# Kernel tuning notes

Hardware: AMD Instinct MI355X
Metric: run time of the kernel (lower is better)

Reference implementation:

```python
import jax, jax.numpy as jnp
import numpy as np

N, E, D, L, G = 100000, 320000, 256, 3, 4096
EPS = 1e-5


def setup_inputs() -> dict:
    key = jax.random.key(0)
    ks = jax.random.split(key, 14)
    s = 0.05
    return {
        "x": jax.random.normal(ks[0], (N, D), jnp.float32),
        "lin1_w": jax.random.normal(ks[1], (L, D, D), jnp.float32) * s,
        "lin1_b": jnp.zeros((L, D), jnp.float32),
        "lin2_w": jax.random.normal(ks[2], (L, D, D), jnp.float32) * s,
        "lin2_b": jnp.zeros((L, D), jnp.float32),
        "bn_g": jnp.ones((L, D), jnp.float32),
        "bn_b": jnp.zeros((L, D), jnp.float32),
        "gru_wih": jax.random.normal(ks[3], (L, 3 * D, D), jnp.float32) * s,
        "gru_whh": jax.random.normal(ks[4], (L, 3 * D, D), jnp.float32) * s,
        "gru_bih": jnp.zeros((L, 3 * D), jnp.float32),
        "gru_bhh": jnp.zeros((L, 3 * D), jnp.float32),
        "ln_g": jnp.ones((D,), jnp.float32),
        "ln_b": jnp.zeros((D,), jnp.float32),
        "edge_index": jax.random.randint(ks[5], (2, E), 0, N),
        "batch": jnp.sort(jax.random.randint(ks[6], (N,), 0, G)),
    }


def _layer_norm(h, g, b):
    mu = jnp.mean(h, axis=-1, keepdims=True)
    var = jnp.mean(jnp.square(h - mu), axis=-1, keepdims=True)
    return (h - mu) * jax.lax.rsqrt(var + EPS) * g + b


def _batch_norm(h, g, b):
    mu = jnp.mean(h, axis=0)
    var = jnp.mean(jnp.square(h - mu), axis=0)
    return (h - mu) * jax.lax.rsqrt(var + EPS) * g + b


def reference(x, lin1_w, lin1_b, lin2_w, lin2_b, bn_g, bn_b,
              gru_wih, gru_whh, gru_bih, gru_bhh, ln_g, ln_b,
              edge_index, batch):
    src, dst = edge_index[0], edge_index[1]
    h = x
    m = jnp.ones((), x.dtype)   # running elementwise product (starts as scalar 1)
    e = jnp.zeros((), x.dtype)  # running elementwise sum (starts as scalar 0)
    hs = []
    for i in range(L):
        # GIN aggregation: (1+eps)*h + sum_{j->i} h_j, eps=0
        agg = jax.ops.segment_sum(h[src], dst, num_segments=N) + h
        # GIN MLP: Linear -> ReLU -> Linear, then outer ReLU
        t = jax.nn.relu(agg @ lin1_w[i].T + lin1_b[i])
        t = t @ lin2_w[i].T + lin2_b[i]
        g = jax.nn.relu(t)
        g = _batch_norm(g, bn_g[i], bn_b[i])  # dropout is identity in eval
        # GRUCell(input=g, hidden=h)
        gi = g @ gru_wih[i].T + gru_bih[i]
        gh = h @ gru_whh[i].T + gru_bhh[i]
        i_r, i_z, i_n = jnp.split(gi, 3, axis=-1)
        h_r, h_z, h_n = jnp.split(gh, 3, axis=-1)
        r = jax.nn.sigmoid(i_r + h_r)
        z = jax.nn.sigmoid(i_z + h_z)
        n = jnp.tanh(i_n + r * h_n)
        h = (1.0 - z) * n + z * h
        h = _layer_norm(h, ln_g, ln_b)
        m = m * h
        e = e + h
        hs.append(h)
    node_rep = jnp.concatenate(hs + [m, e], axis=-1)  # [N, (L+2)*D]
    out = jax.ops.segment_max(node_rep, batch, num_segments=G)  # [G, (L+2)*D]
    return out
```

## Files before the change

kernel.cpp:

```cpp
#include <hip/hip_runtime.h>

#define N_NODES 100000
#define N_EDGES 320000
#define N_GRAPH 4096
#define M_PAD   100096
#define N_TILES 782
#define LN_EPS  1e-5f
#define S_EL    ((size_t)M_PAD * 256)
#define CAP     32

typedef __attribute__((ext_vector_type(8))) short short8;
typedef __attribute__((ext_vector_type(4))) float f32x4;
typedef unsigned short u16;

__device__ __forceinline__ float bf2f(u16 u){
  return __uint_as_float(((unsigned)u) << 16);
}
__device__ __forceinline__ u16 f2bf(float f){
  unsigned u = __float_as_uint(f);
  return (u16)((u + 0x7FFFu + ((u >> 16) & 1u)) >> 16);
}
__device__ __forceinline__ float ldext(const void* p, long i, bool f32){
  return f32 ? ((const float*)p)[i] : bf2f(((const u16*)p)[i]);
}
__device__ __forceinline__ float fsigm(float x){
  return __builtin_amdgcn_rcpf(1.0f + __expf(-x));
}
__device__ __forceinline__ float ftanh(float x){
  float cx = fminf(fmaxf(x, -15.f), 15.f);
  return 1.0f - 2.0f*__builtin_amdgcn_rcpf(__expf(2.0f*cx) + 1.0f);
}

__device__ __forceinline__ int swzb(int row, int colByte){
  return (row << 9) + (colByte ^ ((row & 7) << 4));
}

__global__ void k_detect(const unsigned* __restrict__ x32, int* __restrict__ flag){
  unsigned u = x32[threadIdx.x];
  int ef = (int)((u >> 23) & 0xFFu);
  int ok = (ef >= 64 && ef <= 190) ? 1 : 0;
  #pragma unroll
  for (int o=1; o<64; o<<=1) ok += __shfl_xor(ok, o);
  if (threadIdx.x == 0) *flag = (ok >= 32) ? 1 : 0;
}

__global__ void k_wconv(const void* __restrict__ src, u16* __restrict__ dst,
                        const int* __restrict__ dflag){
  const bool f32 = (*dflag != 0);
  size_t base = ((size_t)blockIdx.x*256 + threadIdx.x)*8;
  if (f32){
    const float* s = (const float*)src + base;
    float4 a = *(const float4*)s;
    float4 b = *(const float4*)(s + 4);
    ushort4 lo = make_ushort4(f2bf(a.x),f2bf(a.y),f2bf(a.z),f2bf(a.w));
    ushort4 hi = make_ushort4(f2bf(b.x),f2bf(b.y),f2bf(b.z),f2bf(b.w));
    uint4 v;
    v.x = (unsigned)lo.x | ((unsigned)lo.y<<16);
    v.y = (unsigned)lo.z | ((unsigned)lo.w<<16);
    v.z = (unsigned)hi.x | ((unsigned)hi.y<<16);
    v.w = (unsigned)hi.z | ((unsigned)hi.w<<16);
    *(uint4*)&dst[base] = v;
  } else {
    *(uint4*)&dst[base] = *(const uint4*)((const u16*)src + base);
  }
}

__global__ void k_h_init(const void* __restrict__ x, u16* __restrict__ h,
                         const int* __restrict__ dflag){
  const bool f32 = (*dflag != 0);
  int i = blockIdx.x*256 + threadIdx.x;
  size_t base = (size_t)i*8;
  int n = (int)(base >> 8);
  uint4 v = make_uint4(0,0,0,0);
  if (n < N_NODES){
    if (f32){
      const float* xf = (const float*)x + base;
      float4 a = *(const float4*)xf;
      float4 b = *(const float4*)(xf + 4);
      ushort4 lo = make_ushort4(f2bf(a.x),f2bf(a.y),f2bf(a.z),f2bf(a.w));
      ushort4 hi = make_ushort4(f2bf(b.x),f2bf(b.y),f2bf(b.z),f2bf(b.w));
      v.x = (unsigned)lo.x | ((unsigned)lo.y<<16);
      v.y = (unsigned)lo.z | ((unsigned)lo.w<<16);
      v.z = (unsigned)hi.x | ((unsigned)hi.y<<16);
      v.w = (unsigned)hi.z | ((unsigned)hi.w<<16);
    } else {
      v = *(const uint4*)((const u16*)x + base);
    }
  }
  *(uint4*)&h[base] = v;
}

__global__ void k_bucket_build(const int* __restrict__ ei, int* __restrict__ cnt,
                               int* __restrict__ bucket, int* __restrict__ ovf,
                               int* __restrict__ ovfcnt){
  int e = blockIdx.x*256 + threadIdx.x;
  if (e >= N_EDGES) return;
  int s = ei[e];
  int d = ei[N_EDGES + e];
  int pos = atomicAdd(&cnt[d], 1);
  if (pos < CAP) bucket[(size_t)d*CAP + pos] = s;
  else { int o = atomicAdd(ovfcnt, 1); ovf[o] = e; }
}

__global__ __launch_bounds__(256) void k_gather(
    const unsigned* __restrict__ h32, const int* __restrict__ cnt,
    const int* __restrict__ bucket, unsigned* __restrict__ G32)
{
  int gid = blockIdx.x*256 + threadIdx.x;
  int n = gid >> 7;
  int j = gid & 127;
  unsigned hv = h32[(size_t)n*128 + j];
  float lo = bf2f((u16)(hv & 0xFFFFu));
  float hi = bf2f((u16)(hv >> 16));
  int c = (n < N_NODES) ? min(cnt[n], CAP) : 0;
  const int* bk = &bucket[(size_t)n*CAP];
  for (int k = 0; k < c; k++){
    int s = bk[k];
    unsigned v = h32[(size_t)s*128 + j];
    lo += bf2f((u16)(v & 0xFFFFu));
    hi += bf2f((u16)(v >> 16));
  }
  G32[(size_t)n*128 + j] = (unsigned)f2bf(lo) | ((unsigned)f2bf(hi) << 16);
}

__global__ void k_ovf_scatter(const unsigned* __restrict__ h32,
                              const int* __restrict__ ei,
                              const int* __restrict__ ovf,
                              const int* __restrict__ ovfcnt,
                              unsigned* __restrict__ G32){
  const long work = (long)(*ovfcnt) * 128;
  for (long i = (long)blockIdx.x*256 + threadIdx.x; i < work;
       i += (long)gridDim.x*256){
    int e = ovf[i >> 7];
    int j = (int)(i & 127);
    int s = ei[e];
    int d = ei[N_EDGES + e];
    unsigned sv = h32[(size_t)s*128 + j];
    float vlo = bf2f((u16)(sv & 0xFFFFu));
    float vhi = bf2f((u16)(sv >> 16));
    unsigned* addr = &G32[(size_t)d*128 + j];
    unsigned old = *addr;
    while (true){
      unsigned assumed = old;
      u16 nl = f2bf(bf2f((u16)(assumed & 0xFFFFu)) + vlo);
      u16 nh = f2bf(bf2f((u16)(assumed >> 16)) + vhi);
      unsigned nv = (unsigned)nl | ((unsigned)nh << 16);
      old = atomicCAS(addr, assumed, nv);
      if (old == assumed) break;
    }
  }
}

__device__ __forceinline__ void stage_tile64(const u16* __restrict__ g,
                                             u16* __restrict__ tile,
                                             size_t rowBase, int tid){
  #pragma unroll
  for (int j=0;j<4;j++){
    int cid = j*512 + tid;
    int r  = cid >> 5;
    int cb = (cid & 31) << 4;
    uint4 v = *(const uint4*)((const char*)g + (((rowBase + r) << 9) + cb));
    *(uint4*)((char*)tile + swzb(r, cb)) = v;
  }
}

__device__ __forceinline__ void stage_tile64_bn(const u16* __restrict__ g,
                                                u16* __restrict__ tile,
                                                size_t rowBase, int tid,
                                                const float* __restrict__ ss){
  #pragma unroll
  for (int j=0;j<4;j++){
    int cid = j*512 + tid;
    int r  = cid >> 5;
    int cb = (cid & 31) << 4;
    uint4 v = *(const uint4*)((const char*)g + (((rowBase + r) << 9) + cb));
    unsigned vv[4] = {v.x, v.y, v.z, v.w};
    uint4 o;
    unsigned* op = (unsigned*)&o;
    #pragma unroll
    for (int q=0;q<4;q++){
      float4 s2 = *(const float4*)&ss[cb + q*4];
      float x0 = bf2f((u16)(vv[q] & 0xFFFFu))*s2.x + s2.y;
      float x1 = bf2f((u16)(vv[q] >> 16))    *s2.z + s2.w;
      op[q] = (unsigned)f2bf(x0) | ((unsigned)f2bf(x1) << 16);
    }
    *(uint4*)((char*)tile + swzb(r, cb)) = o;
  }
}

template<int KT>
__device__ __forceinline__ void gate_gemm(
    f32x4 (&acc)[4][2], const u16* __restrict__ tA1, const u16* __restrict__ tA2,
    const u16* __restrict__ W1, const u16* __restrict__ W2,
    int wc, int fr, int quad)
{
  constexpr int NH = KT/256;
  const size_t wrow0 = (size_t)(wc + fr)*256 + quad*8;
  const size_t wrow1 = (size_t)(wc + 16 + fr)*256 + quad*8;
  short8 bcur0 = *(const short8*)&W1[wrow0];
  short8 bcur1 = *(const short8*)&W1[wrow1];
  #pragma unroll
  for (int h2=0; h2<NH; h2++){
    const u16* tA = h2 ? tA2 : tA1;
    const u16* Wv = h2 ? W2  : W1;
    #pragma unroll
    for (int kk=0; kk<256; kk+=32){
      short8 af[4];
      #pragma unroll
      for (int mi=0;mi<4;mi++)
        af[mi] = *(const short8*)((const char*)tA + swzb(mi*16 + fr, kk*2 + quad*16));
      short8 bn0 = bcur0, bn1 = bcur1;
      const bool last = (kk == 224) && (h2 == NH-1);
      if (!last){
        const u16* Wn = (kk == 224) ? W2 : Wv;
        const int   kn = (kk == 224) ? 0  : kk + 32;
        bn0 = *(const short8*)&Wn[wrow0 + kn];
        bn1 = *(const short8*)&Wn[wrow1 + kn];
      }
      #pragma unroll
      for (int mi=0;mi<4;mi++){
        acc[mi][0] = __builtin_amdgcn_mfma_f32_16x16x32_bf16(af[mi], bcur0, acc[mi][0], 0, 0, 0);
        acc[mi][1] = __builtin_amdgcn_mfma_f32_16x16x32_bf16(af[mi], bcur1, acc[mi][1], 0, 0, 0);
      }
      bcur0 = bn0; bcur1 = bn1;
    }
  }
}

#define ZERO_ACC42(a) { f32x4 _z = {0.f,0.f,0.f,0.f}; \
  _Pragma("unroll") for (int _i=0;_i<4;_i++) \
  _Pragma("unroll") for (int _j=0;_j<2;_j++) a[_i][_j] = _z; }

__global__ __launch_bounds__(512, 2) void k_mlp(
    u16* __restrict__ Gp,
    const u16* __restrict__ w1, const void* __restrict__ b1,
    const u16* __restrict__ w2, const void* __restrict__ b2,
    long bO, float* __restrict__ bns, const int* __restrict__ dflag)
{
  const bool f32 = (*dflag != 0);
  __shared__ u16 Ag[64*256];
  __shared__ u16 At[64*256];
  const int tid = threadIdx.x;
  const size_t rowBase = (size_t)blockIdx.x * 64;
  const int lane = tid & 63, wave = tid >> 6;
  const int wc = wave * 32;
  const int fr = lane & 15, quad = lane >> 4;

  stage_tile64(Gp, Ag, rowBase, tid);
  __syncthreads();

  f32x4 acc[4][2];
  ZERO_ACC42(acc);
  gate_gemm<256>(acc, Ag, nullptr, w1, nullptr, wc, fr, quad);

  #pragma unroll
  for (int ni=0;ni<2;ni++){
    const int col = wc + ni*16 + fr;
    const float bv = ldext(b1, bO + col, f32);
    #pragma unroll
    for (int mi=0;mi<4;mi++)
      #pragma unroll
      for (int r4=0;r4<4;r4++){
        const int row = mi*16 + quad*4 + r4;
        float v = fmaxf(acc[mi][ni][r4] + bv, 0.f);
        *(u16*)((char*)At + swzb(row, col*2)) = f2bf(v);
      }
  }
  __syncthreads();

  ZERO_ACC42(acc);
  gate_gemm<256>(acc, At, nullptr, w2, nullptr, wc, fr, quad);

  #pragma unroll
  for (int ni=0;ni<2;ni++){
    const int col = wc + ni*16 + fr;
    const float bv = ldext(b2, bO + col, f32);
    float s1 = 0.f, s2 = 0.f;
    #pragma unroll
    for (int mi=0;mi<4;mi++)
      #pragma unroll
      for (int r4=0;r4<4;r4++){
        const int row = mi*16 + quad*4 + r4;
        const size_t grow = rowBase + row;
        float v = fmaxf(acc[mi][ni][r4] + bv, 0.f);
        Gp[grow*256 + col] = f2bf(v);
        if (grow < N_NODES){ s1 += v; s2 += v*v; }
      }
    s1 += __shfl_xor(s1, 16); s1 += __shfl_xor(s1, 32);
    s2 += __shfl_xor(s2, 16); s2 += __shfl_xor(s2, 32);
    if (quad == 0){
      unsafeAtomicAdd(&bns[col],       s1);
      unsafeAtomicAdd(&bns[256 + col], s2);
    }
  }
}

__global__ void k_bn_fin(const float* __restrict__ sums,
                         const void* __restrict__ gam, const void* __restrict__ bet,
                         long gO, float* __restrict__ ss,
                         const int* __restrict__ dflag){
  const bool f32 = (*dflag != 0);
  int c = threadIdx.x;
  float mu  = sums[c] * (1.f/N_NODES);
  float var = sums[256 + c] * (1.f/N_NODES) - mu*mu;
  float sc  = ldext(gam, gO + c, f32) * rsqrtf(fmaxf(var, 0.f) + LN_EPS);
  ss[2*c]     = sc;
  ss[2*c + 1] = ldext(bet, gO + c, f32) - mu*sc;
}

__global__ __launch_bounds__(512, 2) void k_gru(
    const u16* __restrict__ Gp, const u16* __restrict__ hp,
    const u16* __restrict__ wihl, const u16* __restrict__ whhl,
    const void* __restrict__ bih, const void* __restrict__ bhh, long bo,
    const void* __restrict__ lng, const void* __restrict__ lnb,
    const float* __restrict__ ss, u16* __restrict__ hout,
    const int* __restrict__ dflag)
{
  const bool f32 = (*dflag != 0);
  __shared__ u16 Ag[64*256];
  __shared__ u16 Ah[64*256];
  const int tid = threadIdx.x;
  const size_t rowBase = (size_t)blockIdx.x * 64;
  const int lane = tid & 63, wave = tid >> 6;
  const int wc = wave * 32;
  const int fr = lane & 15, quad = lane >> 4;

  stage_tile64_bn(Gp, Ag, rowBase, tid, ss);
  stage_tile64(hp, Ah, rowBase, tid);
  __syncthreads();

  f32x4 acc[4][2];
  unsigned pk[4][2][2];

  ZERO_ACC42(acc);
  gate_gemm<256>(acc, Ah, nullptr, whhl + 512*256, nullptr, wc, fr, quad);
  #pragma unroll
  for (int ni=0;ni<2;ni++){
    const float bv = ldext(bhh, bo + 512 + wc + ni*16 + fr, f32);
    #pragma unroll
    for (int mi=0;mi<4;mi++)
      #pragma unroll
      for (int q=0;q<2;q++)
        pk[mi][ni][q] = (unsigned)f2bf(acc[mi][ni][2*q] + bv)
                      | ((unsigned)f2bf(acc[mi][ni][2*q+1] + bv) << 16);
  }

  ZERO_ACC42(acc);
  gate_gemm<512>(acc, Ag, Ah, wihl, whhl, wc, fr, quad);
  #pragma unroll
  for (int ni=0;ni<2;ni++){
    const int col = wc + ni*16 + fr;
    const float bv = ldext(bih, bo + col, f32) + ldext(bhh, bo + col, f32);
    #pragma unroll
    for (int mi=0;mi<4;mi++)
      #pragma unroll
      for (int q=0;q<2;q++){
        float h0 = bf2f((u16)(pk[mi][ni][q] & 0xFFFFu));
        float h1 = bf2f((u16)(pk[mi][ni][q] >> 16));
        float r0 = fsigm(acc[mi][ni][2*q]   + bv);
        float r1 = fsigm(acc[mi][ni][2*q+1] + bv);
        pk[mi][ni][q] = (unsigned)f2bf(r0*h0) | ((unsigned)f2bf(r1*h1) << 16);
      }
  }

  ZERO_ACC42(acc);
  gate_gemm<256>(acc, Ag, nullptr, wihl + 512*256, nullptr, wc, fr, quad);
  #pragma unroll
  for (int ni=0;ni<2;ni++){
    const float bv = ldext(bih, bo + 512 + wc + ni*16 + fr, f32);
    #pragma unroll
    for (int mi=0;mi<4;mi++)
      #pragma unroll
      for (int q=0;q<2;q++){
        float n0 = ftanh(acc[mi][ni][2*q]   + bv + bf2f((u16)(pk[mi][ni][q] & 0xFFFFu)));
        float n1 = ftanh(acc[mi][ni][2*q+1] + bv + bf2f((u16)(pk[mi][ni][q] >> 16)));
        pk[mi][ni][q] = (unsigned)f2bf(n0) | ((unsigned)f2bf(n1) << 16);
      }
  }

  ZERO_ACC42(acc);
  gate_gemm<512>(acc, Ag, Ah, wihl + 256*256, whhl + 256*256, wc, fr, quad);
  #pragma unroll
  for (int ni=0;ni<2;ni++){
    const int col = wc + ni*16 + fr;
    const float bv = ldext(bih, bo + 256 + col, f32) + ldext(bhh, bo + 256 + col, f32);
    #pragma unroll
    for (int mi=0;mi<4;mi++)
      #pragma unroll
      for (int q=0;q<2;q++){
        const int row0 = mi*16 + quad*4 + 2*q;
        const unsigned pv = pk[mi][ni][q];
        float v0, v1;
        {
          const float z = fsigm(acc[mi][ni][2*q] + bv);
          const float hval = bf2f(*(const u16*)((const char*)Ah + swzb(row0, col*2)));
          v0 = (1.f - z)*bf2f((u16)(pv & 0xFFFFu)) + z*hval;
        }
        {
          const float z = fsigm(acc[mi][ni][2*q+1] + bv);
          const float hval = bf2f(*(const u16*)((const char*)Ah + swzb(row0+1, col*2)));
          v1 = (1.f - z)*bf2f((u16)(pv >> 16)) + z*hval;
        }
        pk[mi][ni][q] = (unsigned)f2bf(v0) | ((unsigned)f2bf(v1) << 16);
      }
  }

  __syncthreads();
  #pragma unroll
  for (int ni=0;ni<2;ni++){
    const int col = wc + ni*16 + fr;
    #pragma unroll
    for (int mi=0;mi<4;mi++)
      #pragma unroll
      for (int q=0;q<2;q++){
        const int row0 = mi*16 + quad*4 + 2*q;
        const unsigned pv = pk[mi][ni][q];
        *(u16*)((char*)Ag + swzb(row0,   col*2)) = (u16)(pv & 0xFFFFu);
        *(u16*)((char*)Ag + swzb(row0+1, col*2)) = (u16)(pv >> 16);
      }
  }
  __syncthreads();

  const int erow = tid >> 3, seg = tid & 7;
  float s1 = 0.f, s2 = 0.f;
  #pragma unroll
  for (int jj=0;jj<8;jj++){
    uint2 w = *(const uint2*)((const char*)Ag + swzb(erow, seg*64 + jj*8));
    float v0 = bf2f((u16)(w.x & 0xFFFFu)), v1 = bf2f((u16)(w.x >> 16));
    float v2 = bf2f((u16)(w.y & 0xFFFFu)), v3 = bf2f((u16)(w.y >> 16));
    s1 += v0 + v1 + v2 + v3;
    s2 += v0*v0 + v1*v1 + v2*v2 + v3*v3;
  }
  s1 += __shfl_xor(s1, 1); s2 += __shfl_xor(s2, 1);
  s1 += __shfl_xor(s1, 2); s2 += __shfl_xor(s2, 2);
  s1 += __shfl_xor(s1, 4); s2 += __shfl_xor(s2, 4);
  const float mu   = s1 * (1.f/256.f);
  const float var  = s2 * (1.f/256.f) - mu*mu;
  const float rstd = rsqrtf(fmaxf(var, 0.f) + LN_EPS);

  const size_t rb = (rowBase + erow)*256 + (size_t)seg*32;
  #pragma unroll
  for (int jj=0;jj<8;jj++){
    uint2 w = *(const uint2*)((const char*)Ag + swzb(erow, seg*64 + jj*8));
    const long c0 = seg*32 + jj*4;
    float v0 = (bf2f((u16)(w.x & 0xFFFFu)) - mu)*rstd*ldext(lng, c0+0, f32) + ldext(lnb, c0+0, f32);
    float v1 = (bf2f((u16)(w.x >> 16))     - mu)*rstd*ldext(lng, c0+1, f32) + ldext(lnb, c0+1, f32);
    float v2 = (bf2f((u16)(w.y & 0xFFFFu)) - mu)*rstd*ldext(lng, c0+2, f32) + ldext(lnb, c0+2, f32);
    float v3 = (bf2f((u16)(w.y >> 16))     - mu)*rstd*ldext(lng, c0+3, f32) + ldext(lnb, c0+3, f32);
    *(ushort4*)&hout[rb + jj*4] = make_ushort4(f2bf(v0), f2bf(v1), f2bf(v2), f2bf(v3));
  }
}

__global__ __launch_bounds__(256) void k_segmax(
    const u16* __restrict__ plane, void* __restrict__ out, long slice,
    const int* __restrict__ batch, const int* __restrict__ dflag)
{
  const bool f32 = (*dflag != 0);
  const int g = blockIdx.x*4 + (threadIdx.x >> 6);
  const int lane = threadIdx.x & 63;
  int lo = 0, hi = N_NODES;
  while (lo < hi){ int mid = (lo + hi) >> 1; if (batch[mid] < g) lo = mid + 1; else hi = mid; }
  const int s = lo;
  hi = N_NODES;
  while (lo < hi){ int mid = (lo + hi) >> 1; if (batch[mid] < g + 1) lo = mid + 1; else hi = mid; }
  const int epos = lo;

  const float NINF = __uint_as_float(0xFF800000u);
  float a0=NINF, a1=NINF, a2=NINF, a3=NINF;
  for (int r = s; r < epos; r++){
    ushort4 v = *(const ushort4*)&plane[(size_t)r*256 + lane*4];
    a0 = fmaxf(a0, bf2f(v.x)); a1 = fmaxf(a1, bf2f(v.y));
    a2 = fmaxf(a2, bf2f(v.z)); a3 = fmaxf(a3, bf2f(v.w));
  }
  const long ob = (long)g*1280 + slice + lane*4;
  if (f32){
    float* o = (float*)out + ob;
    o[0]=a0; o[1]=a1; o[2]=a2; o[3]=a3;
  } else {
    *(ushort4*)((u16*)out + ob) = make_ushort4(f2bf(a0), f2bf(a1), f2bf(a2), f2bf(a3));
  }
}

__global__ __launch_bounds__(256) void k_segmax_me(
    const u16* __restrict__ h0, const u16* __restrict__ h1,
    const u16* __restrict__ h2, void* __restrict__ out,
    const int* __restrict__ batch, const int* __restrict__ dflag)
{
  const bool f32 = (*dflag != 0);
  const int g = blockIdx.x*4 + (threadIdx.x >> 6);
  const int lane = threadIdx.x & 63;
  int lo = 0, hi = N_NODES;
  while (lo < hi){ int mid = (lo + hi) >> 1; if (batch[mid] < g) lo = mid + 1; else hi = mid; }
  const int s = lo;
  hi = N_NODES;
  while (lo < hi){ int mid = (lo + hi) >> 1; if (batch[mid] < g + 1) lo = mid + 1; else hi = mid; }
  const int epos = lo;

  const float NINF = __uint_as_float(0xFF800000u);
  float m0=NINF,m1=NINF,m2=NINF,m3=NINF;
  float e0=NINF,e1=NINF,e2=NINF,e3=NINF;
  for (int r = s; r < epos; r++){
    const size_t rb = (size_t)r*256 + lane*4;
    ushort4 a = *(const ushort4*)&h0[rb];
    ushort4 b = *(const ushort4*)&h1[rb];
    ushort4 c = *(const ushort4*)&h2[rb];
    float a0=bf2f(a.x),a1=bf2f(a.y),a2=bf2f(a.z),a3=bf2f(a.w);
    float b0=bf2f(b.x),b1=bf2f(b.y),b2=bf2f(b.z),b3=bf2f(b.w);
    float c0=bf2f(c.x),c1=bf2f(c.y),c2=bf2f(c.z),c3=bf2f(c.w);
    m0=fmaxf(m0,a0*b0*c0); m1=fmaxf(m1,a1*b1*c1);
    m2=fmaxf(m2,a2*b2*c2); m3=fmaxf(m3,a3*b3*c3);
    e0=fmaxf(e0,a0+b0+c0); e1=fmaxf(e1,a1+b1+c1);
    e2=fmaxf(e2,a2+b2+c2); e3=fmaxf(e3,a3+b3+c3);
  }
  const long obm = (long)g*1280 + 768  + lane*4;
  const long obe = (long)g*1280 + 1024 + lane*4;
  if (f32){
    float* o = (float*)out;
    o[obm+0]=m0; o[obm+1]=m1; o[obm+2]=m2; o[obm+3]=m3;
    o[obe+0]=e0; o[obe+1]=e1; o[obe+2]=e2; o[obe+3]=e3;
  } else {
    *(ushort4*)((u16*)out + obm) = make_ushort4(f2bf(m0), f2bf(m1), f2bf(m2), f2bf(m3));
    *(ushort4*)((u16*)out + obe) = make_ushort4(f2bf(e0), f2bf(e1), f2bf(e2), f2bf(e3));
  }
}

extern "C" void kernel_launch(void* const* d_in, const int* in_sizes, int n_in,
                              void* d_out, int out_size, void* d_ws, size_t ws_size,
                              hipStream_t stream)
{
  const void* x   = d_in[0];
  const void* l1w = d_in[1];  const void* l1b = d_in[2];
  const void* l2w = d_in[3];  const void* l2b = d_in[4];
  const void* bng = d_in[5];  const void* bnb = d_in[6];
  const void* wih = d_in[7];  const void* whh = d_in[8];
  const void* bih = d_in[9];  const void* bhh = d_in[10];
  const void* lng = d_in[11]; const void* lnb = d_in[12];
  const int* ei    = (const int*)d_in[13];
  const int* batch = (const int*)d_in[14];
  (void)in_sizes; (void)n_in; (void)out_size; (void)ws_size;

  const size_t PL = S_EL * 2;
  char* p = (char*)d_ws; size_t off = 0;
  auto take = [&](size_t b){ void* q = p + off; off += (b + 255) & ~(size_t)255; return q; };
  u16*      hx   = (u16*)take(PL);
  u16*      hA   = (u16*)take(PL);
  u16*      hB   = (u16*)take(PL);
  u16*      G    = (u16*)take(PL);
  float*    bns  = (float*)take(512*4);
  float*    bss  = (float*)take(512*4);
  int*      dflg = (int*)take(256);
  int*      cnt  = (int*)take((size_t)N_NODES*4);
  int*      bkt  = (int*)take((size_t)N_NODES*CAP*4);
  int*      ovf  = (int*)take((size_t)N_EDGES*4);
  int*      ovfc = (int*)take(256);
  u16*      wb1  = (u16*)take((size_t)3*65536*2);
  u16*      wb2  = (u16*)take((size_t)3*65536*2);
  u16*      wbih = (u16*)take((size_t)3*196608*2);
  u16*      wbhh = (u16*)take((size_t)3*196608*2);

  k_detect<<<1, 64, 0, stream>>>((const unsigned*)x, dflg);
  hipMemsetAsync(cnt, 0, (size_t)N_NODES*4, stream);
  hipMemsetAsync(ovfc, 0, 4, stream);
  k_h_init <<<S_EL/8/256, 256, 0, stream>>>(x, hx, dflg);
  k_bucket_build<<<(N_EDGES + 255)/256, 256, 0, stream>>>(ei, cnt, bkt, ovf, ovfc);
  k_wconv<<< 96, 256, 0, stream>>>(l1w, wb1,  dflg);
  k_wconv<<< 96, 256, 0, stream>>>(l2w, wb2,  dflg);
  k_wconv<<<288, 256, 0, stream>>>(wih, wbih, dflg);
  k_wconv<<<288, 256, 0, stream>>>(whh, wbhh, dflg);

  const u16* hin[3]  = {hx, hA, hB};
  u16*       hout[3] = {hA, hB, hx};

  for (int l = 0; l < 3; l++){
    const long bo = (long)l*768;
    hipMemsetAsync(bns, 0, 512*4, stream);
    k_gather<<<(M_PAD*128)/256, 256, 0, stream>>>((const unsigned*)hin[l], cnt, bkt, (unsigned*)G);
    k_ovf_scatter<<<512, 256, 0, stream>>>((const unsigned*)hin[l], ei, ovf, ovfc, (unsigned*)G);

    k_mlp<<<N_TILES*2, 512, 0, stream>>>(G, wb1 + (size_t)l*65536, l1b,
                                         wb2 + (size_t)l*65536, l2b,
                                         (long)l*256, bns, dflg);
    k_bn_fin<<<1, 256, 0, stream>>>(bns, bng, bnb, (long)l*256, bss, dflg);

    k_gru<<<N_TILES*2, 512, 0, stream>>>(G, hin[l],
                                         wbih + (size_t)l*196608, wbhh + (size_t)l*196608,
                                         bih, bhh, bo, lng, lnb, bss, hout[l], dflg);

    k_segmax<<<N_GRAPH/4, 256, 0, stream>>>(hout[l], d_out, (long)l*256, batch, dflg);
  }
  k_segmax_me<<<N_GRAPH/4, 256, 0, stream>>>(hA, hB, hx, d_out, batch, dflg);
}
```

Measured before the change: 1.639 ms.

## Fuse per-layer segment max into one final kernel and prefetch A fragments

Removes the three per-layer segment-max launches and computes the max of h0, h1, h2, their product and their sum in a single final kernel. That kernel reads the three hidden planes once and binary-searches each graph's node range once instead of four times. Separately, the gate GEMM now prefetches the next A fragments from shared memory alongside the next B weights, double-buffering both operands so LDS latency overlaps the MFMAs. The cost is higher register pressure in the GEMM and a somewhat heavier reduction kernel.

Result: faster. 1.567 ms (-4.4%).

```diff
diff --git a/kernel.cpp b/kernel.cpp
--- a/kernel.cpp
+++ b/kernel.cpp
@@ -197,32 +197,38 @@
   constexpr int NH = KT/256;
   const size_t wrow0 = (size_t)(wc + fr)*256 + quad*8;
   const size_t wrow1 = (size_t)(wc + 16 + fr)*256 + quad*8;
+  short8 acur[4];
+  #pragma unroll
+  for (int mi=0;mi<4;mi++)
+    acur[mi] = *(const short8*)((const char*)tA1 + swzb(mi*16 + fr, quad*16));
   short8 bcur0 = *(const short8*)&W1[wrow0];
   short8 bcur1 = *(const short8*)&W1[wrow1];
   #pragma unroll
   for (int h2=0; h2<NH; h2++){
-    const u16* tA = h2 ? tA2 : tA1;
-    const u16* Wv = h2 ? W2  : W1;
     #pragma unroll
     for (int kk=0; kk<256; kk+=32){
-      short8 af[4];
-      #pragma unroll
-      for (int mi=0;mi<4;mi++)
-        af[mi] = *(const short8*)((const char*)tA + swzb(mi*16 + fr, kk*2 + quad*16));
-      short8 bn0 = bcur0, bn1 = bcur1;
       const bool last = (kk == 224) && (h2 == NH-1);
+      short8 an[4], bn0, bn1;
       if (!last){
-        const u16* Wn = (kk == 224) ? W2 : Wv;
+        const u16* tAn = (kk == 224) ? tA2 : (h2 ? tA2 : tA1);
+        const u16* Wn  = (kk == 224) ? W2  : (h2 ? W2  : W1);
         const int   kn = (kk == 224) ? 0  : kk + 32;
+        #pragma unroll
+        for (int mi=0;mi<4;mi++)
+          an[mi] = *(const short8*)((const char*)tAn + swzb(mi*16 + fr, kn*2 + quad*16));
         bn0 = *(const short8*)&Wn[wrow0 + kn];
         bn1 = *(const short8*)&Wn[wrow1 + kn];
       }
       #pragma unroll
       for (int mi=0;mi<4;mi++){
-        acc[mi][0] = __builtin_amdgcn_mfma_f32_16x16x32_bf16(af[mi], bcur0, acc[mi][0], 0, 0, 0);
-        acc[mi][1] = __builtin_amdgcn_mfma_f32_16x16x32_bf16(af[mi], bcur1, acc[mi][1], 0, 0, 0);
-      }
-      bcur0 = bn0; bcur1 = bn1;
+        acc[mi][0] = __builtin_amdgcn_mfma_f32_16x16x32_bf16(acur[mi], bcur0, acc[mi][0], 0, 0, 0);
+        acc[mi][1] = __builtin_amdgcn_mfma_f32_16x16x32_bf16(acur[mi], bcur1, acc[mi][1], 0, 0, 0);
+      }
+      if (!last){
+        #pragma unroll
+        for (int mi=0;mi<4;mi++) acur[mi] = an[mi];
+        bcur0 = bn0; bcur1 = bn1;
+      }
     }
   }
 }
@@ -451,37 +457,7 @@
   }
 }
 
-__global__ __launch_bounds__(256) void k_segmax(
-    const u16* __restrict__ plane, void* __restrict__ out, long slice,
-    const int* __restrict__ batch, const int* __restrict__ dflag)
-{
-  const bool f32 = (*dflag != 0);
-  const int g = blockIdx.x*4 + (threadIdx.x >> 6);
-  const int lane = threadIdx.x & 63;
-  int lo = 0, hi = N_NODES;
-  while (lo < hi){ int mid = (lo + hi) >> 1; if (batch[mid] < g) lo = mid + 1; else hi = mid; }
-  const int s = lo;
-  hi = N_NODES;
-  while (lo < hi){ int mid = (lo + hi) >> 1; if (batch[mid] < g + 1) lo = mid + 1; else hi = mid; }
-  const int epos = lo;
-
-  const float NINF = __uint_as_float(0xFF800000u);
-  float a0=NINF, a1=NINF, a2=NINF, a3=NINF;
-  for (int r = s; r < epos; r++){
-    ushort4 v = *(const ushort4*)&plane[(size_t)r*256 + lane*4];
-    a0 = fmaxf(a0, bf2f(v.x)); a1 = fmaxf(a1, bf2f(v.y));
-    a2 = fmaxf(a2, bf2f(v.z)); a3 = fmaxf(a3, bf2f(v.w));
-  }
-  const long ob = (long)g*1280 + slice + lane*4;
-  if (f32){
-    float* o = (float*)out + ob;
-    o[0]=a0; o[1]=a1; o[2]=a2; o[3]=a3;
-  } else {
-    *(ushort4*)((u16*)out + ob) = make_ushort4(f2bf(a0), f2bf(a1), f2bf(a2), f2bf(a3));
-  }
-}
-
-__global__ __launch_bounds__(256) void k_segmax_me(
+__global__ __launch_bounds__(256) void k_segmax_all(
     const u16* __restrict__ h0, const u16* __restrict__ h1,
     const u16* __restrict__ h2, void* __restrict__ out,
     const int* __restrict__ batch, const int* __restrict__ dflag)
@@ -497,30 +473,44 @@
   const int epos = lo;
 
   const float NINF = __uint_as_float(0xFF800000u);
-  float m0=NINF,m1=NINF,m2=NINF,m3=NINF;
-  float e0=NINF,e1=NINF,e2=NINF,e3=NINF;
+  float x0[4], x1[4], x2[4], mm[4], ee[4];
+  #pragma unroll
+  for (int j=0;j<4;j++){ x0[j]=NINF; x1[j]=NINF; x2[j]=NINF; mm[j]=NINF; ee[j]=NINF; }
   for (int r = s; r < epos; r++){
     const size_t rb = (size_t)r*256 + lane*4;
     ushort4 a = *(const ushort4*)&h0[rb];
     ushort4 b = *(const ushort4*)&h1[rb];
     ushort4 c = *(const ushort4*)&h2[rb];
-    float a0=bf2f(a.x),a1=bf2f(a.y),a2=bf2f(a.z),a3=bf2f(a.w);
-    float b0=bf2f(b.x),b1=bf2f(b.y),b2=bf2f(b.z),b3=bf2f(b.w);
-    float c0=bf2f(c.x),c1=bf2f(c.y),c2=bf2f(c.z),c3=bf2f(c.w);
-    m0=fmaxf(m0,a0*b0*c0); m1=fmaxf(m1,a1*b1*c1);
-    m2=fmaxf(m2,a2*b2*c2); m3=fmaxf(m3,a3*b3*c3);
-    e0=fmaxf(e0,a0+b0+c0); e1=fmaxf(e1,a1+b1+c1);
-    e2=fmaxf(e2,a2+b2+c2); e3=fmaxf(e3,a3+b3+c3);
-  }
-  const long obm = (long)g*1280 + 768  + lane*4;
-  const long obe = (long)g*1280 + 1024 + lane*4;
+    float av[4] = {bf2f(a.x),bf2f(a.y),bf2f(a.z),bf2f(a.w)};
+    float bv[4] = {bf2f(b.x),bf2f(b.y),bf2f(b.z),bf2f(b.w)};
+    float cv[4] = {bf2f(c.x),bf2f(c.y),bf2f(c.z),bf2f(c.w)};
+    #pragma unroll
+    for (int j=0;j<4;j++){
+      x0[j] = fmaxf(x0[j], av[j]);
+      x1[j] = fmaxf(x1[j], bv[j]);
+      x2[j] = fmaxf(x2[j], cv[j]);
+      mm[j] = fmaxf(mm[j], av[j]*bv[j]*cv[j]);
+      ee[j] = fmaxf(ee[j], av[j]+bv[j]+cv[j]);
+    }
+  }
+  const long ob = (long)g*1280 + lane*4;
   if (f32){
     float* o = (float*)out;
-    o[obm+0]=m0; o[obm+1]=m1; o[obm+2]=m2; o[obm+3]=m3;
-    o[obe+0]=e0; o[obe+1]=e1; o[obe+2]=e2; o[obe+3]=e3;
+    #pragma unroll
+    for (int j=0;j<4;j++){
+      o[ob +        j] = x0[j];
+      o[ob +  256 + j] = x1[j];
+      o[ob +  512 + j] = x2[j];
+      o[ob +  768 + j] = mm[j];
+      o[ob + 1024 + j] = ee[j];
+    }
   } else {
-    *(ushort4*)((u16*)out + obm) = make_ushort4(f2bf(m0), f2bf(m1), f2bf(m2), f2bf(m3));
-    *(ushort4*)((u16*)out + obe) = make_ushort4(f2bf(e0), f2bf(e1), f2bf(e2), f2bf(e3));
+    u16* o = (u16*)out;
+    *(ushort4*)&o[ob]        = make_ushort4(f2bf(x0[0]), f2bf(x0[1]), f2bf(x0[2]), f2bf(x0[3]));
+    *(ushort4*)&o[ob +  256] = make_ushort4(f2bf(x1[0]), f2bf(x1[1]), f2bf(x1[2]), f2bf(x1[3]));
+    *(ushort4*)&o[ob +  512] = make_ushort4(f2bf(x2[0]), f2bf(x2[1]), f2bf(x2[2]), f2bf(x2[3]));
+    *(ushort4*)&o[ob +  768] = make_ushort4(f2bf(mm[0]), f2bf(mm[1]), f2bf(mm[2]), f2bf(mm[3]));
+    *(ushort4*)&o[ob + 1024] = make_ushort4(f2bf(ee[0]), f2bf(ee[1]), f2bf(ee[2]), f2bf(ee[3]));
   }
 }
 
@@ -585,8 +575,6 @@
     k_gru<<<N_TILES*2, 512, 0, stream>>>(G, hin[l],
                                          wbih + (size_t)l*196608, wbhh + (size_t)l*196608,
                                          bih, bhh, bo, lng, lnb, bss, hout[l], dflg);
-
-    k_segmax<<<N_GRAPH/4, 256, 0, stream>>>(hout[l], d_out, (long)l*256, batch, dflg);
-  }
-  k_segmax_me<<<N_GRAPH/4, 256, 0, stream>>>(hA, hB, hx, d_out, batch, dflg);
-}
+  }
+  k_segmax_all<<<N_GRAPH/4, 256, 0, stream>>>(hA, hB, hx, d_out, batch, dflg);
+}
```
